# Optimization experiments

Measured on AMD Instinct MI355X. Metric: run time of the kernel, lower is better.

## Reference

```python
import jax, jax.numpy as jnp
import numpy as np

EPS = 1e-7  # Keras K.epsilon()


def setup_inputs() -> dict:
    key = jax.random.key(0)
    ks = jax.random.split(key, 8)
    B, T, D = 64, 2048, 256
    context = jax.random.normal(ks[0], (B, T, D), dtype=jnp.float32)
    aspect = jax.random.normal(ks[1], (B, D), dtype=jnp.float32)
    sentence = jax.random.normal(ks[2], (B, D), dtype=jnp.float32)
    context_mask = jax.random.randint(ks[3], (B, T), 0, 2).astype(bool)
    context_w = jax.random.normal(ks[4], (D, D), dtype=jnp.float32) * 0.05
    aspect_w = jax.random.normal(ks[5], (D, D), dtype=jnp.float32) * 0.05
    sent_w = jax.random.normal(ks[6], (D, D), dtype=jnp.float32) * 0.05
    attend_w = jax.random.normal(ks[7], (D, 1), dtype=jnp.float32) * 0.05
    return {"context": context, "aspect": aspect, "sentence": sentence,
            "context_mask": context_mask, "context_w": context_w,
            "aspect_w": aspect_w, "sent_w": sent_w, "attend_w": attend_w}


def reference(context, aspect, sentence, context_mask, context_w, aspect_w, sent_w, attend_w):
    # bias term from aspect/sentence, broadcast over time instead of K.repeat: [B,1,D]
    bias = (aspect @ aspect_w + sentence @ sent_w)[:, None, :]
    h = jnp.tanh(jnp.einsum('btd,de->bte', context, context_w) + bias)  # [B,T,D]
    g = jnp.einsum('btd,d->bt', h, attend_w[:, 0])                      # [B,T]
    a = jnp.exp(g) * context_mask.astype(jnp.float32)                   # faithful: no max-subtract
    a = a / (jnp.sum(a, axis=-1, keepdims=True) + EPS)
    attend_context = jnp.einsum('btd,bt->bd', context, a) + sentence     # [B,D]
    return attend_context
```

## Files before the change

kernel.cpp:

```cpp
#include <hip/hip_runtime.h>
#include <hip/hip_bf16.h>

#define BB  64
#define TT  2048
#define DD  256
#define EPSV 1e-7f
#define TILE_R 32
#define NTILE  8
#define NBLK   512

typedef __attribute__((ext_vector_type(8))) short bf16x8;
typedef __attribute__((ext_vector_type(4))) float f32x4;

__device__ __forceinline__ ushort f2bf(float f) {
    union { float f; unsigned u; } v; v.f = f;
    unsigned u = v.u;
    unsigned r = (u + 0x7FFFu + ((u >> 16) & 1u)) >> 16;
    return (ushort)r;
}

__device__ __forceinline__ float bf2f(unsigned h16) {
    union { unsigned u; float f; } v; v.u = h16 << 16;
    return v.f;
}

__device__ __forceinline__ unsigned pkbf(float lo, float hi) {
    union { float f; unsigned u; } a, b;
    a.f = lo; b.f = hi;
    return __builtin_amdgcn_perm(b.u + 0x8000u, a.u + 0x8000u, 0x07060302u);
}

__device__ __forceinline__ float tanh_fast(float x) {
    float e = __expf(2.0f * x);
    return 1.0f - 2.0f * __builtin_amdgcn_rcpf(e + 1.0f);
}

template<int CTRL>
__device__ __forceinline__ float dpp_rot_add(float x) {
    union { float f; int i; } a; a.f = x;
    int r = __builtin_amdgcn_update_dpp(0, a.i, CTRL, 0xF, 0xF, true);
    union { int i; float f; } b; b.i = r;
    return x + b.f;
}
__device__ __forceinline__ float row16_sum(float x) {
    x = dpp_rot_add<0x121>(x);
    x = dpp_rot_add<0x122>(x);
    x = dpp_rot_add<0x124>(x);
    x = dpp_rot_add<0x128>(x);
    return x;
}

__global__ __launch_bounds__(256) void prep_kernel(
    const float* __restrict__ aspect, const float* __restrict__ sentence,
    const float* __restrict__ context_w, const float* __restrict__ aspect_w,
    const float* __restrict__ sent_w,
    float* __restrict__ bias_part, ushort* __restrict__ wfrag_ws)
{
    const int blk = blockIdx.x, tid = threadIdx.x;
    if (blk < 512) {
        const int b = blk >> 3, q = blk & 7, e = tid;
        float s = 0.f;
        #pragma unroll 4
        for (int dd = 0; dd < 32; ++dd) {
            const int d = q * 32 + dd;
            s = fmaf(aspect[b * DD + d],   aspect_w[d * DD + e], s);
            s = fmaf(sentence[b * DD + d], sent_w[d * DD + e],   s);
        }
        bias_part[blk * DD + e] = s;
    } else {
        const int flat = (blk - 512) * 256 + tid;
        const int lane = flat & 63;
        const int kn   = flat >> 6;
        const int kk   = kn >> 4;
        const int n    = kn & 15;
        const int krow = kk * 32 + ((lane >> 4) << 3);
        const int col  = n * 16 + (lane & 15);
        bf16x8 v;
        #pragma unroll
        for (int j = 0; j < 8; ++j)
            v[j] = (short)f2bf(context_w[(size_t)(krow + j) * DD + col]);
        *reinterpret_cast<bf16x8*>(wfrag_ws + (size_t)flat * 8) = v;
    }
}

__global__ __launch_bounds__(512, 2) void attn_main(
    const float* __restrict__ ctx, const int* __restrict__ mask,
    const float* __restrict__ attend_w,
    const float* __restrict__ bias_part, const ushort* __restrict__ wfrag_ws,
    float* __restrict__ partial_ws, float* __restrict__ esum_ws)
{
    __shared__ __align__(16) char bfb[2][TILE_R * 512];
    __shared__ float bias_lds[256];
    __shared__ float aw_lds[256];
    __shared__ float mask_lds[256];
    __shared__ float gpart[TILE_R][8];
    __shared__ float esw[8];
    __shared__ float part_d[8][256];

    const int tid  = threadIdx.x;
    const int wave = tid >> 6;
    const int lane = tid & 63;
    const int blk  = blockIdx.x;
    const int b    = blk >> 3;
    const int cg   = wave;

    if (tid < 256) {
        float bs = 0.f;
        #pragma unroll
        for (int q = 0; q < 8; ++q) bs += bias_part[(b * 8 + q) * DD + tid];
        bias_lds[tid] = bs;
    } else {
        const int m = tid - 256;
        aw_lds[m]   = attend_w[m];
        mask_lds[m] = (float)mask[blk * 256 + m];
    }

    bf16x8 Bf[8][2];
    {
        const bf16x8* wf = reinterpret_cast<const bf16x8*>(wfrag_ws);
        #pragma unroll
        for (int kk = 0; kk < 8; ++kk) {
            Bf[kk][0] = wf[(kk * 16 + cg * 2 + 0) * 64 + lane];
            Bf[kk][1] = wf[(kk * 16 + cg * 2 + 1) * 64 + lane];
        }
    }

    const float4* src = reinterpret_cast<const float4*>(ctx);

    {
        const size_t base4 = (size_t)(blk * NTILE) * 2048;
        char* dst = bfb[0];
        #pragma unroll
        for (int i = 0; i < 4; ++i) {
            const int idx = i * 512 + tid;
            const float4 v = src[base4 + idx];
            const int row = idx >> 6, c4 = idx & 63;
            uint2 u; u.x = pkbf(v.x, v.y); u.y = pkbf(v.z, v.w);
            *reinterpret_cast<uint2*>(dst + row * 512 + ((c4 * 8) ^ ((row & 7) << 4))) = u;
        }
    }
    __syncthreads();

    float accd[4] = {0.f, 0.f, 0.f, 0.f};
    float es_tot = 0.f;

    for (int it = 0; it < NTILE; ++it) {
        const int cur = it & 1;
        const char* lb = bfb[cur];

        float4 sreg[4];
        if (it + 1 < NTILE) {
            const size_t base4 = (size_t)(blk * NTILE + it + 1) * 2048;
            #pragma unroll
            for (int i = 0; i < 4; ++i) sreg[i] = src[base4 + i * 512 + tid];
        }

        f32x4 acc[2][2];
        #pragma unroll
        for (int rt = 0; rt < 2; ++rt) {
            acc[rt][0] = (f32x4){0.f, 0.f, 0.f, 0.f};
            acc[rt][1] = (f32x4){0.f, 0.f, 0.f, 0.f};
        }
        #pragma unroll
        for (int rt = 0; rt < 2; ++rt) {
            const int row = rt * 16 + (lane & 15);
            const char* ab = lb + row * 512;
            const int asw = (row & 7) << 4;
            #pragma unroll
            for (int kk = 0; kk < 8; ++kk) {
                const bf16x8 a = *reinterpret_cast<const bf16x8*>(
                    ab + ((kk * 64 + ((lane >> 4) << 4)) ^ asw));
                acc[rt][0] = __builtin_amdgcn_mfma_f32_16x16x32_bf16(a, Bf[kk][0], acc[rt][0], 0, 0, 0);
                acc[rt][1] = __builtin_amdgcn_mfma_f32_16x16x32_bf16(a, Bf[kk][1], acc[rt][1], 0, 0, 0);
            }
        }

        {
            const int c0 = cg * 32 + (lane & 15), c1 = c0 + 16;
            const float bs0 = bias_lds[c0], aw0 = aw_lds[c0];
            const float bs1 = bias_lds[c1], aw1 = aw_lds[c1];
            #pragma unroll
            for (int rt = 0; rt < 2; ++rt) {
                #pragma unroll
                for (int j = 0; j < 4; ++j) {
                    float gv = tanh_fast(acc[rt][0][j] + bs0) * aw0
                             + tanh_fast(acc[rt][1][j] + bs1) * aw1;
                    gv = row16_sum(gv);
                    if ((lane & 15) == 0)
                        gpart[rt * 16 + ((lane >> 4) << 2) + j][cg] = gv;
                }
            }
        }
        __syncthreads();

        #pragma unroll
        for (int rr = 0; rr < 4; ++rr) {
            const int r = wave * 4 + rr;
            const float4 g0 = *reinterpret_cast<const float4*>(&gpart[r][0]);
            const float4 g1 = *reinterpret_cast<const float4*>(&gpart[r][4]);
            const float g = ((g0.x + g0.y) + (g0.z + g0.w))
                          + ((g1.x + g1.y) + (g1.z + g1.w));
            const float ev = __expf(g) * mask_lds[it * TILE_R + r];
            es_tot += ev;
            const uint2 hv = *reinterpret_cast<const uint2*>(
                lb + r * 512 + ((lane * 8) ^ ((r & 7) << 4)));
            accd[0] = fmaf(bf2f(hv.x & 0xffffu), ev, accd[0]);
            accd[1] = fmaf(bf2f(hv.x >> 16),     ev, accd[1]);
            accd[2] = fmaf(bf2f(hv.y & 0xffffu), ev, accd[2]);
            accd[3] = fmaf(bf2f(hv.y >> 16),     ev, accd[3]);
        }

        if (it + 1 < NTILE) {
            char* dst = bfb[cur ^ 1];
            #pragma unroll
            for (int i = 0; i < 4; ++i) {
                const int idx = i * 512 + tid;
                const int row = idx >> 6, c4 = idx & 63;
                uint2 u; u.x = pkbf(sreg[i].x, sreg[i].y); u.y = pkbf(sreg[i].z, sreg[i].w);
                *reinterpret_cast<uint2*>(dst + row * 512 + ((c4 * 8) ^ ((row & 7) << 4))) = u;
            }
        }
        __syncthreads();
    }

    *reinterpret_cast<float4*>(&part_d[wave][lane * 4]) =
        (float4){accd[0], accd[1], accd[2], accd[3]};
    if (lane == 0) esw[wave] = es_tot;
    __syncthreads();
    if (tid < 256) {
        float s = 0.f;
        #pragma unroll
        for (int w = 0; w < 8; ++w) s += part_d[w][tid];
        partial_ws[blk * DD + tid] = s;
    }
    if (tid == 0) {
        float e = 0.f;
        #pragma unroll
        for (int w = 0; w < 8; ++w) e += esw[w];
        esum_ws[blk] = e;
    }
}

__global__ __launch_bounds__(256) void finalize_kernel(
    const float* __restrict__ sentence, const float* __restrict__ partial_ws,
    const float* __restrict__ esum_ws, float* __restrict__ out)
{
    const int b = blockIdx.x, d = threadIdx.x;
    float es = 0.f, s = 0.f;
    #pragma unroll
    for (int i = 0; i < 8; ++i) {
        es += esum_ws[b * 8 + i];
        s  += partial_ws[(size_t)(b * 8 + i) * DD + d];
    }
    out[b * DD + d] = s / (es + EPSV) + sentence[b * DD + d];
}

extern "C" void kernel_launch(void* const* d_in, const int* in_sizes, int n_in,
                              void* d_out, int out_size, void* d_ws, size_t ws_size,
                              hipStream_t stream)
{
    const float* ctx       = (const float*)d_in[0];
    const float* aspect    = (const float*)d_in[1];
    const float* sentence  = (const float*)d_in[2];
    const int*   mask      = (const int*)  d_in[3];
    const float* context_w = (const float*)d_in[4];
    const float* aspect_w  = (const float*)d_in[5];
    const float* sent_w    = (const float*)d_in[6];
    const float* attend_w  = (const float*)d_in[7];
    float* out = (float*)d_out;

    char* ws = (char*)d_ws;
    ushort* wfrag_ws   = (ushort*)(ws);
    float*  bias_part  = (float*) (ws + 131072);
    float*  esum_ws    = (float*) (ws + 131072 + 524288);
    float*  partial_ws = (float*) (ws + 131072 + 524288 + 2048);

    prep_kernel<<<544, 256, 0, stream>>>(aspect, sentence, context_w, aspect_w, sent_w,
                                         bias_part, wfrag_ws);
    attn_main<<<NBLK, 512, 0, stream>>>(ctx, mask, attend_w, bias_part, wfrag_ws,
                                        partial_ws, esum_ws);
    finalize_kernel<<<BB, 256, 0, stream>>>(sentence, partial_ws, esum_ws, out);
}
```

Baseline: 50.84 us.

## Triple-buffer context tiles with two-ahead prefetch and one barrier per tile

Moves from double to triple LDS buffering. Global loads are prefetched two tiles ahead, and the bf16 conversion plus LDS store for the next tile happens at the top of each iteration, which removes the second __syncthreads per tile. The per-row score partials are stored transposed and double-buffered. Each wave now computes all 32 row exponentials once and broadcasts them with shuffles, and the exp-sum reduction is done within a wave. The costs are more LDS and register pressure from the extra buffer and the longer-lived prefetch registers, which could lower occupancy at the 512x2 launch bounds.

```diff
diff --git a/kernel.cpp b/kernel.cpp
--- a/kernel.cpp
+++ b/kernel.cpp
@@ -89,12 +89,11 @@
     const float* __restrict__ bias_part, const ushort* __restrict__ wfrag_ws,
     float* __restrict__ partial_ws, float* __restrict__ esum_ws)
 {
-    __shared__ __align__(16) char bfb[2][TILE_R * 512];
+    __shared__ __align__(16) char bfb[3][TILE_R * 512];
+    __shared__ float gpartT[2][8][TILE_R];
     __shared__ float bias_lds[256];
     __shared__ float aw_lds[256];
     __shared__ float mask_lds[256];
-    __shared__ float gpart[TILE_R][8];
-    __shared__ float esw[8];
     __shared__ float part_d[8][256];
 
     const int tid  = threadIdx.x;
@@ -126,33 +125,74 @@
     }
 
     const float4* src = reinterpret_cast<const float4*>(ctx);
-
+    const int cc  = tid;
+    const int crow0 = cc >> 5,        c80 = cc & 31;
+    const int crow1 = (512 + cc) >> 5, c81 = (512 + cc) & 31;
+
+    float4 sreg[4];
     {
         const size_t base4 = (size_t)(blk * NTILE) * 2048;
+        #pragma unroll
+        for (int i = 0; i < 2; ++i) {
+            const int c = i * 512 + tid;
+            sreg[2 * i + 0] = src[base4 + 2 * c + 0];
+            sreg[2 * i + 1] = src[base4 + 2 * c + 1];
+        }
         char* dst = bfb[0];
         #pragma unroll
-        for (int i = 0; i < 4; ++i) {
-            const int idx = i * 512 + tid;
-            const float4 v = src[base4 + idx];
-            const int row = idx >> 6, c4 = idx & 63;
-            uint2 u; u.x = pkbf(v.x, v.y); u.y = pkbf(v.z, v.w);
-            *reinterpret_cast<uint2*>(dst + row * 512 + ((c4 * 8) ^ ((row & 7) << 4))) = u;
+        for (int i = 0; i < 2; ++i) {
+            const int row = i ? crow1 : crow0, c8 = i ? c81 : c80;
+            uint4 u;
+            u.x = pkbf(sreg[2 * i].x,     sreg[2 * i].y);
+            u.y = pkbf(sreg[2 * i].z,     sreg[2 * i].w);
+            u.z = pkbf(sreg[2 * i + 1].x, sreg[2 * i + 1].y);
+            u.w = pkbf(sreg[2 * i + 1].z, sreg[2 * i + 1].w);
+            *reinterpret_cast<uint4*>(dst + row * 512 + ((c8 * 16) ^ ((row & 7) << 4))) = u;
+        }
+        const size_t b1 = base4 + 2048;
+        #pragma unroll
+        for (int i = 0; i < 2; ++i) {
+            const int c = i * 512 + tid;
+            sreg[2 * i + 0] = src[b1 + 2 * c + 0];
+            sreg[2 * i + 1] = src[b1 + 2 * c + 1];
         }
     }
     __syncthreads();
 
+    const int c0 = cg * 32 + (lane & 15), c1 = c0 + 16;
+    const float bs0 = bias_lds[c0], awc0 = aw_lds[c0];
+    const float bs1 = bias_lds[c1], awc1 = aw_lds[c1];
+
     float accd[4] = {0.f, 0.f, 0.f, 0.f};
-    float es_tot = 0.f;
+    float es_acc = 0.f;
+    int cb = 0;
 
     for (int it = 0; it < NTILE; ++it) {
-        const int cur = it & 1;
-        const char* lb = bfb[cur];
-
-        float4 sreg[4];
+        const int nb = (cb == 2) ? 0 : cb + 1;
+        const int gp = it & 1;
+        const char* lb = bfb[cb];
+
         if (it + 1 < NTILE) {
-            const size_t base4 = (size_t)(blk * NTILE + it + 1) * 2048;
+            char* dst = bfb[nb];
             #pragma unroll
-            for (int i = 0; i < 4; ++i) sreg[i] = src[base4 + i * 512 + tid];
+            for (int i = 0; i < 2; ++i) {
+                const int row = i ? crow1 : crow0, c8 = i ? c81 : c80;
+                uint4 u;
+                u.x = pkbf(sreg[2 * i].x,     sreg[2 * i].y);
+                u.y = pkbf(sreg[2 * i].z,     sreg[2 * i].w);
+                u.z = pkbf(sreg[2 * i + 1].x, sreg[2 * i + 1].y);
+                u.w = pkbf(sreg[2 * i + 1].z, sreg[2 * i + 1].w);
+                *reinterpret_cast<uint4*>(dst + row * 512 + ((c8 * 16) ^ ((row & 7) << 4))) = u;
+            }
+        }
+        if (it + 2 < NTILE) {
+            const size_t base4 = (size_t)(blk * NTILE + it + 2) * 2048;
+            #pragma unroll
+            for (int i = 0; i < 2; ++i) {
+                const int c = i * 512 + tid;
+                sreg[2 * i + 0] = src[base4 + 2 * c + 0];
+                sreg[2 * i + 1] = src[base4 + 2 * c + 1];
+            }
         }
 
         f32x4 acc[2][2];
@@ -175,57 +215,47 @@
             }
         }
 
-        {
-            const int c0 = cg * 32 + (lane & 15), c1 = c0 + 16;
-            const float bs0 = bias_lds[c0], aw0 = aw_lds[c0];
-            const float bs1 = bias_lds[c1], aw1 = aw_lds[c1];
-            #pragma unroll
-            for (int rt = 0; rt < 2; ++rt) {
-                #pragma unroll
-                for (int j = 0; j < 4; ++j) {
-                    float gv = tanh_fast(acc[rt][0][j] + bs0) * aw0
-                             + tanh_fast(acc[rt][1][j] + bs1) * aw1;
-                    gv = row16_sum(gv);
-                    if ((lane & 15) == 0)
-                        gpart[rt * 16 + ((lane >> 4) << 2) + j][cg] = gv;
-                }
+        #pragma unroll
+        for (int rt = 0; rt < 2; ++rt) {
+            float g0 = row16_sum(tanh_fast(acc[rt][0][0] + bs0) * awc0
+                               + tanh_fast(acc[rt][1][0] + bs1) * awc1);
+            float g1 = row16_sum(tanh_fast(acc[rt][0][1] + bs0) * awc0
+                               + tanh_fast(acc[rt][1][1] + bs1) * awc1);
+            float g2 = row16_sum(tanh_fast(acc[rt][0][2] + bs0) * awc0
+                               + tanh_fast(acc[rt][1][2] + bs1) * awc1);
+            float g3 = row16_sum(tanh_fast(acc[rt][0][3] + bs0) * awc0
+                               + tanh_fast(acc[rt][1][3] + bs1) * awc1);
+            if ((lane & 15) == 0) {
+                const int r = rt * 16 + ((lane >> 4) << 2);
+                *reinterpret_cast<float4*>(&gpartT[gp][cg][r]) = (float4){g0, g1, g2, g3};
             }
         }
         __syncthreads();
+
+        const int erow = lane & 31;
+        float gsum = 0.f;
+        #pragma unroll
+        for (int c = 0; c < 8; ++c) gsum += gpartT[gp][c][erow];
+        const float ev = __expf(gsum) * mask_lds[it * TILE_R + erow];
+        es_acc += (lane < 32) ? ev : 0.f;
 
         #pragma unroll
         for (int rr = 0; rr < 4; ++rr) {
             const int r = wave * 4 + rr;
-            const float4 g0 = *reinterpret_cast<const float4*>(&gpart[r][0]);
-            const float4 g1 = *reinterpret_cast<const float4*>(&gpart[r][4]);
-            const float g = ((g0.x + g0.y) + (g0.z + g0.w))
-                          + ((g1.x + g1.y) + (g1.z + g1.w));
-            const float ev = __expf(g) * mask_lds[it * TILE_R + r];
-            es_tot += ev;
+            const float e = __shfl(ev, r);
             const uint2 hv = *reinterpret_cast<const uint2*>(
                 lb + r * 512 + ((lane * 8) ^ ((r & 7) << 4)));
-            accd[0] = fmaf(bf2f(hv.x & 0xffffu), ev, accd[0]);
-            accd[1] = fmaf(bf2f(hv.x >> 16),     ev, accd[1]);
-            accd[2] = fmaf(bf2f(hv.y & 0xffffu), ev, accd[2]);
-            accd[3] = fmaf(bf2f(hv.y >> 16),     ev, accd[3]);
-        }
-
-        if (it + 1 < NTILE) {
-            char* dst = bfb[cur ^ 1];
-            #pragma unroll
-            for (int i = 0; i < 4; ++i) {
-                const int idx = i * 512 + tid;
-                const int row = idx >> 6, c4 = idx & 63;
-                uint2 u; u.x = pkbf(sreg[i].x, sreg[i].y); u.y = pkbf(sreg[i].z, sreg[i].w);
-                *reinterpret_cast<uint2*>(dst + row * 512 + ((c4 * 8) ^ ((row & 7) << 4))) = u;
-            }
-        }
-        __syncthreads();
+            accd[0] = fmaf(bf2f(hv.x & 0xffffu), e, accd[0]);
+            accd[1] = fmaf(bf2f(hv.x >> 16),     e, accd[1]);
+            accd[2] = fmaf(bf2f(hv.y & 0xffffu), e, accd[2]);
+            accd[3] = fmaf(bf2f(hv.y >> 16),     e, accd[3]);
+        }
+
+        cb = nb;
     }
 
     *reinterpret_cast<float4*>(&part_d[wave][lane * 4]) =
         (float4){accd[0], accd[1], accd[2], accd[3]};
-    if (lane == 0) esw[wave] = es_tot;
     __syncthreads();
     if (tid < 256) {
         float s = 0.f;
@@ -233,11 +263,10 @@
         for (int w = 0; w < 8; ++w) s += part_d[w][tid];
         partial_ws[blk * DD + tid] = s;
     }
-    if (tid == 0) {
-        float e = 0.f;
-        #pragma unroll
-        for (int w = 0; w < 8; ++w) e += esw[w];
-        esum_ws[blk] = e;
+    if (wave == 0) {
+        float s = row16_sum(es_acc);
+        s += __shfl_xor(s, 16);
+        if (lane == 0) esum_ws[blk] = s;
     }
 }
 
```

Result: faster. 46.89 us (-7.8%).
